# Performance work log

Hardware: AMD Instinct MI355X
Metric: run time of the kernel (lower is better)

## Reference

```python
import jax, jax.numpy as jnp
import numpy as np

N = 50000   # num nodes
E = 800000  # num edges (avg degree 16)
D = 64      # feature dim for input and both layers


def setup_inputs() -> dict:
    key = jax.random.key(0)
    ks = jax.random.split(key, 8)
    x = jax.random.normal(ks[0], (N, D), dtype=jnp.float32)
    edge_index = jax.random.randint(ks[1], (2, E), 0, N, dtype=jnp.int32)
    s = 1.0 / np.sqrt(D)
    # PyG SAGEConv params per layer: lin_l (on aggregated neighbors, with bias),
    # lin_r (on root node, no bias)
    Wl0 = jax.random.uniform(ks[2], (D, D), jnp.float32, -s, s)
    bl0 = jax.random.uniform(ks[3], (D,), jnp.float32, -s, s)
    Wr0 = jax.random.uniform(ks[4], (D, D), jnp.float32, -s, s)
    Wl1 = jax.random.uniform(ks[5], (D, D), jnp.float32, -s, s)
    bl1 = jax.random.uniform(ks[6], (D,), jnp.float32, -s, s)
    Wr1 = jax.random.uniform(ks[7], (D, D), jnp.float32, -s, s)
    return dict(node_features=x, edge_index=edge_index,
                Wl0=Wl0, bl0=bl0, Wr0=Wr0, Wl1=Wl1, bl1=bl1, Wr1=Wr1)


def _sage_conv(x, src, dst, Wl, bl, Wr):
    """PyG SAGEConv (mean aggr) after add_self_loops: mean over neighbors+self."""
    msg = x[src]  # [E, D] irregular gather
    summ = jax.ops.segment_sum(msg, dst, num_segments=x.shape[0]) + x  # self-loop
    deg = jax.ops.segment_sum(jnp.ones(src.shape, x.dtype), dst,
                              num_segments=x.shape[0]) + 1.0
    mean = summ / deg[:, None]
    return mean @ Wl + bl + x @ Wr


def reference(node_features, edge_index, Wl0, bl0, Wr0, Wl1, bl1, Wr1):
    src, dst = edge_index[0], edge_index[1]
    # dropout is a no-op in eval mode; batch_norms are unused in the original forward
    x = jax.nn.relu(_sage_conv(node_features, src, dst, Wl0, bl0, Wr0))
    x = jax.nn.relu(_sage_conv(x, src, dst, Wl1, bl1, Wr1))
    return x
```

## Files before the change

kernel.cpp:

```cpp
#include <hip/hip_runtime.h>
#include <hip/hip_bf16.h>

#define N_NODES 50000
#define N_EDGES 800000
#define FDIM 64
#define NBUCK 196
#define CAP 4608
#define PAD 16

typedef __attribute__((ext_vector_type(8))) short short8;
typedef __attribute__((ext_vector_type(4))) float f32x4;

__device__ __forceinline__ unsigned f2bf(float f) {
    unsigned u = __float_as_uint(f);
    u += 0x7fffu + ((u >> 16) & 1u);
    return u >> 16;
}
__device__ __forceinline__ float bf2f_lo(unsigned u) { return __uint_as_float(u << 16); }
__device__ __forceinline__ float bf2f_hi(unsigned u) { return __uint_as_float(u & 0xffff0000u); }

__device__ __forceinline__ int excl_scan_256(int v, int* wtot, int* wincl) {
    const int t = threadIdx.x, lane = t & 63, w = t >> 6;
    int sv = v;
#pragma unroll
    for (int off = 1; off < 64; off <<= 1) {
        int u = __shfl_up(sv, off, 64);
        if (lane >= off) sv += u;
    }
    if (lane == 63) wtot[w] = sv;
    __syncthreads();
    if (w == 0 && lane < 4) {
        int incl = 0;
#pragma unroll
        for (int k = 0; k < 4; ++k)
            if (k <= lane) incl += wtot[k];
        wincl[lane] = incl;
    }
    __syncthreads();
    return (w ? wincl[w - 1] : 0) + sv - v;
}

__global__ __launch_bounds__(256)
void preprocess_kernel(const float* __restrict__ x0, unsigned short* __restrict__ x_bf,
                       const float* __restrict__ Wl0, const float* __restrict__ Wr0,
                       const float* __restrict__ Wl1, const float* __restrict__ Wr1,
                       unsigned short* __restrict__ pW, int* __restrict__ cur_pad) {
    const int b = blockIdx.x;
    const int t = threadIdx.x;
    if (b < 3125) {
        int i = (b * 256 + t) * 4;
        float4 v = *(const float4*)(x0 + i);
        uint2 o;
        o.x = f2bf(v.x) | (f2bf(v.y) << 16);
        o.y = f2bf(v.z) | (f2bf(v.w) << 16);
        *(uint2*)(x_bf + i) = o;
    } else if (b < 3129) {
        const float* Wsrc[4] = {Wl0, Wr0, Wl1, Wr1};
        const float* W = Wsrc[b - 3125];
        unsigned short* P = pW + (b - 3125) * FDIM * FDIM;
        for (int idx = t; idx < FDIM * FDIM; idx += 256) {
            int j = idx & 7;
            int lane = (idx >> 3) & 63;
            int g = idx >> 9;
            int ct = g >> 1, kk = g & 1;
            int k = kk * 32 + ((lane >> 4) & 3) * 8 + j;
            int col = ct * 16 + (lane & 15);
            P[idx] = (unsigned short)f2bf(W[k * FDIM + col]);
        }
    } else {
        if (t < NBUCK) cur_pad[t * PAD] = 0;
    }
}

__global__ __launch_bounds__(256)
void bucket_scatter_kernel(const int* __restrict__ src, const int* __restrict__ dst,
                           int* __restrict__ cur_pad, unsigned* __restrict__ ebuf) {
    __shared__ int h[NBUCK];
    __shared__ int base[NBUCK];
    const int t = threadIdx.x;

    if (t < NBUCK) h[t] = 0;
    __syncthreads();

    int e0 = blockIdx.x * 1024;
    int bk[4], rk[4]; unsigned pk[4];
#pragma unroll
    for (int k = 0; k < 4; ++k) {
        int e = e0 + k * 256 + t;
        if (e < N_EDGES) {
            int d = dst[e];
            bk[k] = d >> 8;
            pk[k] = ((unsigned)d << 16) | (unsigned)src[e];
            rk[k] = atomicAdd(&h[bk[k]], 1);
        } else bk[k] = -1;
    }
    __syncthreads();
    if (t < NBUCK) {
        int c = h[t];
        base[t] = c ? (t * CAP + atomicAdd(&cur_pad[t * PAD], c)) : 0;
    }
    __syncthreads();
#pragma unroll
    for (int k = 0; k < 4; ++k)
        if (bk[k] >= 0) ebuf[base[bk[k]] + rk[k]] = pk[k];
}

__global__ __launch_bounds__(256)
void bucket_csr_kernel(const unsigned* __restrict__ ebuf, const int* __restrict__ cur_pad,
                       int* __restrict__ row_start, unsigned short* __restrict__ degs,
                       unsigned short* __restrict__ csr) {
    __shared__ int cnt[256];
    __shared__ int cur[256];
    __shared__ int wtot[4], wincl[4];
    const int b = blockIdx.x;
    const int t = threadIdx.x;
    const int s = b * CAP;
    const int e = s + cur_pad[b * PAD];

    cnt[t] = 0;
    __syncthreads();
    for (int i = s + t; i < e; i += 256)
        atomicAdd(&cnt[(ebuf[i] >> 16) & 255], 1);
    __syncthreads();

    int c = cnt[t];
    int ex = excl_scan_256(c, wtot, wincl);
    cur[t] = ex;
    int node = b * 256 + t;
    if (node < N_NODES) {
        row_start[node] = s + ex;
        degs[node] = (unsigned short)c;
    }
    __syncthreads();

    for (int i = s + t; i < e; i += 256) {
        unsigned pk = ebuf[i];
        int pos = s + atomicAdd(&cur[(pk >> 16) & 255], 1);
        csr[pos] = (unsigned short)pk;
    }
}

template <bool OUT_BF16>
__global__ __launch_bounds__(128)
void sage_fused_kernel(const unsigned short* __restrict__ xb,
                       const int* __restrict__ row_start,
                       const unsigned short* __restrict__ degs,
                       const unsigned short* __restrict__ csr,
                       const unsigned short* __restrict__ pWl,
                       const float* __restrict__ bl,
                       const unsigned short* __restrict__ pWr,
                       float* __restrict__ out_f32,
                       unsigned short* __restrict__ out_bf) {
    __shared__ __align__(16) unsigned short smean[16][FDIM];
    __shared__ __align__(16) unsigned short sxs[16][FDIM];

    const int w = threadIdx.x >> 6;
    const int lane = threadIdx.x & 63;
    const int slot = lane >> 3;
    const int c = lane & 7;
    const int base = blockIdx.x * 16;
    const int r = w * 8 + slot;
    const int n = base + r;

    const int rs = row_start[n];
    const int deg = degs[n];
    const int po = (c ^ (r & 7)) * 8;

    uint4 sv = *(const uint4*)(xb + (size_t)n * FDIM + c * 8);
    *(uint4*)(&sxs[r][po]) = sv;
    float s0 = bf2f_lo(sv.x), s1 = bf2f_hi(sv.x);
    float s2 = bf2f_lo(sv.y), s3 = bf2f_hi(sv.y);
    float s4 = bf2f_lo(sv.z), s5 = bf2f_hi(sv.z);
    float s6 = bf2f_lo(sv.w), s7 = bf2f_hi(sv.w);

#define ACC(v_) do {                                   \
        s0 += bf2f_lo(v_.x); s1 += bf2f_hi(v_.x);      \
        s2 += bf2f_lo(v_.y); s3 += bf2f_hi(v_.y);      \
        s4 += bf2f_lo(v_.z); s5 += bf2f_hi(v_.z);      \
        s6 += bf2f_lo(v_.w); s7 += bf2f_hi(v_.w);      \
    } while (0)

    int idx = rs;
    int rem = deg;
    while (rem >= 4) {
        int a0 = csr[idx + 0];
        int a1 = csr[idx + 1];
        int a2 = csr[idx + 2];
        int a3 = csr[idx + 3];
        uint4 v0 = *(const uint4*)(xb + (size_t)a0 * FDIM + c * 8);
        uint4 v1 = *(const uint4*)(xb + (size_t)a1 * FDIM + c * 8);
        uint4 v2 = *(const uint4*)(xb + (size_t)a2 * FDIM + c * 8);
        uint4 v3 = *(const uint4*)(xb + (size_t)a3 * FDIM + c * 8);
        ACC(v0); ACC(v1); ACC(v2); ACC(v3);
        idx += 4; rem -= 4;
    }
    while (rem > 0) {
        int a0 = csr[idx];
        uint4 v0 = *(const uint4*)(xb + (size_t)a0 * FDIM + c * 8);
        ACC(v0);
        ++idx; --rem;
    }
#undef ACC

    const float inv = 1.0f / (float)(deg + 1);
    uint4 o;
    o.x = f2bf(s0 * inv) | (f2bf(s1 * inv) << 16);
    o.y = f2bf(s2 * inv) | (f2bf(s3 * inv) << 16);
    o.z = f2bf(s4 * inv) | (f2bf(s5 * inv) << 16);
    o.w = f2bf(s6 * inv) | (f2bf(s7 * inv) << 16);
    *(uint4*)(&smean[r][po]) = o;
    __syncthreads();

    const int qq = lane >> 4;
    const int rr = lane & 15;

    short8 am0 = *(const short8*)(&smean[rr][((0 + qq) ^ (rr & 7)) * 8]);
    short8 am1 = *(const short8*)(&smean[rr][((4 + qq) ^ (rr & 7)) * 8]);
    short8 ax0 = *(const short8*)(&sxs[rr][((0 + qq) ^ (rr & 7)) * 8]);
    short8 ax1 = *(const short8*)(&sxs[rr][((4 + qq) ^ (rr & 7)) * 8]);

    const short8* pl = (const short8*)pWl;
    const short8* pr = (const short8*)pWr;

#pragma unroll
    for (int tk = 0; tk < 2; ++tk) {
        const int ct = w * 2 + tk;
        short8 bl0v = pl[(ct * 2 + 0) * 64 + lane];
        short8 bl1v = pl[(ct * 2 + 1) * 64 + lane];
        short8 br0v = pr[(ct * 2 + 0) * 64 + lane];
        short8 br1v = pr[(ct * 2 + 1) * 64 + lane];

        float b = bl[ct * 16 + rr];
        f32x4 acc = {b, b, b, b};
        acc = __builtin_amdgcn_mfma_f32_16x16x32_bf16(am0, bl0v, acc, 0, 0, 0);
        acc = __builtin_amdgcn_mfma_f32_16x16x32_bf16(am1, bl1v, acc, 0, 0, 0);
        acc = __builtin_amdgcn_mfma_f32_16x16x32_bf16(ax0, br0v, acc, 0, 0, 0);
        acc = __builtin_amdgcn_mfma_f32_16x16x32_bf16(ax1, br1v, acc, 0, 0, 0);

#pragma unroll
        for (int reg = 0; reg < 4; ++reg) {
            int node = base + qq * 4 + reg;
            float v = fmaxf(acc[reg], 0.0f);
            if (OUT_BF16) out_bf[(size_t)node * FDIM + ct * 16 + rr] = (unsigned short)f2bf(v);
            else          out_f32[(size_t)node * FDIM + ct * 16 + rr] = v;
        }
    }
}

extern "C" void kernel_launch(void* const* d_in, const int* in_sizes, int n_in,
                              void* d_out, int out_size, void* d_ws, size_t ws_size,
                              hipStream_t stream) {
    const float* x0  = (const float*)d_in[0];
    const int*   ei  = (const int*)d_in[1];
    const float* Wl0 = (const float*)d_in[2];
    const float* bl0 = (const float*)d_in[3];
    const float* Wr0 = (const float*)d_in[4];
    const float* Wl1 = (const float*)d_in[5];
    const float* bl1 = (const float*)d_in[6];
    const float* Wr1 = (const float*)d_in[7];
    float* out = (float*)d_out;

    const int* src = ei;
    const int* dst = ei + N_EDGES;

    int* cur_pad    = (int*)d_ws;
    int* row_start  = cur_pad + 3136;
    unsigned short* degs = (unsigned short*)(row_start + 50000);
    unsigned* ebuf  = (unsigned*)(degs + 50000);
    unsigned short* csr_u16 = (unsigned short*)(ebuf + NBUCK * CAP);
    unsigned short* x_bf = csr_u16 + NBUCK * CAP;
    unsigned short* h_bf = x_bf + (size_t)N_NODES * FDIM;
    unsigned short* pW   = h_bf + (size_t)N_NODES * FDIM;

    preprocess_kernel<<<3130, 256, 0, stream>>>(x0, x_bf, Wl0, Wr0, Wl1, Wr1,
                                                pW, cur_pad);
    bucket_scatter_kernel<<<(N_EDGES + 1023) / 1024, 256, 0, stream>>>(
        src, dst, cur_pad, ebuf);
    bucket_csr_kernel<<<NBUCK, 256, 0, stream>>>(ebuf, cur_pad, row_start, degs, csr_u16);

    sage_fused_kernel<true><<<N_NODES / 16, 128, 0, stream>>>(
        x_bf, row_start, degs, csr_u16, pW + 0 * FDIM * FDIM, bl0,
        pW + 1 * FDIM * FDIM, nullptr, h_bf);
    sage_fused_kernel<false><<<N_NODES / 16, 128, 0, stream>>>(
        h_bf, row_start, degs, csr_u16, pW + 2 * FDIM * FDIM, bl1,
        pW + 3 * FDIM * FDIM, out, nullptr);
}
```

Baseline: 156.7 us.

## Fuse edge bucket scatter into preprocess kernel and unroll gather loop by eight

The bucket scatter step now runs as extra blocks of the preprocess kernel, which removes one kernel launch. The bucket counters are zeroed with a memset beforehand, since the scatter blocks would otherwise race with the block that used to clear them. The neighbor gather loop in the fused SAGE kernel is unrolled to 8 loads per iteration to keep more memory requests in flight. The trade is an added memset launch and higher register pressure in the gather loop.

```diff
diff --git a/kernel.cpp b/kernel.cpp
--- a/kernel.cpp
+++ b/kernel.cpp
@@ -44,7 +44,9 @@
 void preprocess_kernel(const float* __restrict__ x0, unsigned short* __restrict__ x_bf,
                        const float* __restrict__ Wl0, const float* __restrict__ Wr0,
                        const float* __restrict__ Wl1, const float* __restrict__ Wr1,
-                       unsigned short* __restrict__ pW, int* __restrict__ cur_pad) {
+                       unsigned short* __restrict__ pW,
+                       const int* __restrict__ src, const int* __restrict__ dst,
+                       int* __restrict__ cur_pad, unsigned* __restrict__ ebuf) {
     const int b = blockIdx.x;
     const int t = threadIdx.x;
     if (b < 3125) {
@@ -68,41 +70,33 @@
             P[idx] = (unsigned short)f2bf(W[k * FDIM + col]);
         }
     } else {
-        if (t < NBUCK) cur_pad[t * PAD] = 0;
-    }
-}
-
-__global__ __launch_bounds__(256)
-void bucket_scatter_kernel(const int* __restrict__ src, const int* __restrict__ dst,
-                           int* __restrict__ cur_pad, unsigned* __restrict__ ebuf) {
-    __shared__ int h[NBUCK];
-    __shared__ int base[NBUCK];
-    const int t = threadIdx.x;
-
-    if (t < NBUCK) h[t] = 0;
-    __syncthreads();
-
-    int e0 = blockIdx.x * 1024;
-    int bk[4], rk[4]; unsigned pk[4];
-#pragma unroll
-    for (int k = 0; k < 4; ++k) {
-        int e = e0 + k * 256 + t;
-        if (e < N_EDGES) {
-            int d = dst[e];
-            bk[k] = d >> 8;
-            pk[k] = ((unsigned)d << 16) | (unsigned)src[e];
-            rk[k] = atomicAdd(&h[bk[k]], 1);
-        } else bk[k] = -1;
-    }
-    __syncthreads();
-    if (t < NBUCK) {
-        int c = h[t];
-        base[t] = c ? (t * CAP + atomicAdd(&cur_pad[t * PAD], c)) : 0;
-    }
-    __syncthreads();
-#pragma unroll
-    for (int k = 0; k < 4; ++k)
-        if (bk[k] >= 0) ebuf[base[bk[k]] + rk[k]] = pk[k];
+        __shared__ int h[NBUCK];
+        __shared__ int base[NBUCK];
+        if (t < NBUCK) h[t] = 0;
+        __syncthreads();
+
+        int e0 = (b - 3129) * 1024;
+        int bk[4], rk[4]; unsigned pk[4];
+#pragma unroll
+        for (int k = 0; k < 4; ++k) {
+            int e = e0 + k * 256 + t;
+            if (e < N_EDGES) {
+                int d = dst[e];
+                bk[k] = d >> 8;
+                pk[k] = ((unsigned)d << 16) | (unsigned)src[e];
+                rk[k] = atomicAdd(&h[bk[k]], 1);
+            } else bk[k] = -1;
+        }
+        __syncthreads();
+        if (t < NBUCK) {
+            int c = h[t];
+            base[t] = c ? (t * CAP + atomicAdd(&cur_pad[t * PAD], c)) : 0;
+        }
+        __syncthreads();
+#pragma unroll
+        for (int k = 0; k < 4; ++k)
+            if (bk[k] >= 0) ebuf[base[bk[k]] + rk[k]] = pk[k];
+    }
 }
 
 __global__ __launch_bounds__(256)
@@ -182,7 +176,28 @@
 
     int idx = rs;
     int rem = deg;
-    while (rem >= 4) {
+    while (rem >= 8) {
+        int a0 = csr[idx + 0];
+        int a1 = csr[idx + 1];
+        int a2 = csr[idx + 2];
+        int a3 = csr[idx + 3];
+        int a4 = csr[idx + 4];
+        int a5 = csr[idx + 5];
+        int a6 = csr[idx + 6];
+        int a7 = csr[idx + 7];
+        uint4 v0 = *(const uint4*)(xb + (size_t)a0 * FDIM + c * 8);
+        uint4 v1 = *(const uint4*)(xb + (size_t)a1 * FDIM + c * 8);
+        uint4 v2 = *(const uint4*)(xb + (size_t)a2 * FDIM + c * 8);
+        uint4 v3 = *(const uint4*)(xb + (size_t)a3 * FDIM + c * 8);
+        uint4 v4 = *(const uint4*)(xb + (size_t)a4 * FDIM + c * 8);
+        uint4 v5 = *(const uint4*)(xb + (size_t)a5 * FDIM + c * 8);
+        uint4 v6 = *(const uint4*)(xb + (size_t)a6 * FDIM + c * 8);
+        uint4 v7 = *(const uint4*)(xb + (size_t)a7 * FDIM + c * 8);
+        ACC(v0); ACC(v1); ACC(v2); ACC(v3);
+        ACC(v4); ACC(v5); ACC(v6); ACC(v7);
+        idx += 8; rem -= 8;
+    }
+    if (rem >= 4) {
         int a0 = csr[idx + 0];
         int a1 = csr[idx + 1];
         int a2 = csr[idx + 2];
@@ -272,10 +287,9 @@
     unsigned short* h_bf = x_bf + (size_t)N_NODES * FDIM;
     unsigned short* pW   = h_bf + (size_t)N_NODES * FDIM;
 
-    preprocess_kernel<<<3130, 256, 0, stream>>>(x0, x_bf, Wl0, Wr0, Wl1, Wr1,
-                                                pW, cur_pad);
-    bucket_scatter_kernel<<<(N_EDGES + 1023) / 1024, 256, 0, stream>>>(
-        src, dst, cur_pad, ebuf);
+    hipMemsetAsync(cur_pad, 0, 3136 * sizeof(int), stream);
+    preprocess_kernel<<<3911, 256, 0, stream>>>(x0, x_bf, Wl0, Wr0, Wl1, Wr1,
+                                                pW, src, dst, cur_pad, ebuf);
     bucket_csr_kernel<<<NBUCK, 256, 0, stream>>>(ebuf, cur_pad, row_start, degs, csr_u16);
 
     sage_fused_kernel<true><<<N_NODES / 16, 128, 0, stream>>>(
```

Measured after the change: 157.3 us. Within noise of the previous version (+0.4%).
